# Kernel optimization log

Hardware: AMD Instinct MI355X
Metric: run time of the kernel (lower is better)

The kernel has to match this reference:

```python
import jax, jax.numpy as jnp
import numpy as np

T, D, H, B = 2048, 1152, 16, 8
DH = D // H  # 72


def _apply_rope(x, cos_h, sin_h):
    # x: [T, H, DH]; cos_h, sin_h: [T, DH//2] (already chunked halves)
    c = jnp.concatenate([cos_h, cos_h], axis=-1)[:, None, :]  # [T,1,DH]
    s = jnp.concatenate([sin_h, sin_h], axis=-1)[:, None, :]
    x1, x2 = jnp.split(x, 2, axis=-1)
    rot = jnp.concatenate([-x2, x1], axis=-1)
    return x * c + rot * s


def setup_inputs() -> dict:
    key = jax.random.key(0)
    ks = jax.random.split(key, 12)
    hidden_states = jax.random.normal(ks[0], (T, D), jnp.float32)
    inner = jnp.sort(jax.random.randint(ks[1], (B - 1,), 1, T))
    cu_seqlens = jnp.concatenate(
        [jnp.zeros((1,), jnp.int32), inner.astype(jnp.int32), jnp.full((1,), T, jnp.int32)])
    cos = jax.random.uniform(ks[2], (T, DH), jnp.float32, -1.0, 1.0)
    sin = jax.random.uniform(ks[3], (T, DH), jnp.float32, -1.0, 1.0)
    std = 0.02
    Wq = jax.random.normal(ks[4], (D, D), jnp.float32) * std
    Wk = jax.random.normal(ks[5], (D, D), jnp.float32) * std
    Wv = jax.random.normal(ks[6], (D, D), jnp.float32) * std
    Wo = jax.random.normal(ks[7], (D, D), jnp.float32) * std
    bq = jnp.zeros((D,), jnp.float32)
    bk = jnp.zeros((D,), jnp.float32)
    bv = jnp.zeros((D,), jnp.float32)
    bo = jnp.zeros((D,), jnp.float32)
    return {"hidden_states": hidden_states, "cu_seqlens": cu_seqlens,
            "cos": cos, "sin": sin,
            "Wq": Wq, "bq": bq, "Wk": Wk, "bk": bk,
            "Wv": Wv, "bv": bv, "Wo": Wo, "bo": bo}


def reference(hidden_states, cu_seqlens, cos, sin, Wq, bq, Wk, bk, Wv, bv, Wo, bo):
    t = hidden_states.shape[0]
    scale = DH ** -0.5
    q = (hidden_states @ Wq.T + bq).reshape(t, H, DH)
    k = (hidden_states @ Wk.T + bk).reshape(t, H, DH)
    v = (hidden_states @ Wv.T + bv).reshape(t, H, DH)
    # RoPE: cos/sin [T, DH] are chunked in half along last dim, first half used
    cos_h = cos[:, : DH // 2]
    sin_h = sin[:, : DH // 2]
    q = _apply_rope(q, cos_h, sin_h)
    k = _apply_rope(k, cos_h, sin_h)
    # segment ids from cu_seqlens -> block-diagonal (varlen) attention mask
    pos = jnp.arange(t)
    seg = jnp.searchsorted(cu_seqlens, pos, side='right') - 1  # [T]
    mask = seg[:, None] == seg[None, :]  # [T, T]
    scores = jnp.einsum('thd,shd->hts', q, k) * scale  # [H, T, T]
    scores = jnp.where(mask[None], scores, jnp.float32(-1e30))
    attn = jax.nn.softmax(scores, axis=-1)
    out = jnp.einsum('hts,shd->thd', attn, v).reshape(t, D)
    return out @ Wo.T + bo
```

## Files before the change

kernel.cpp:

```cpp
#include <hip/hip_runtime.h>

#define TT 2048
#define DM 1152
#define NHEAD 16
#define HDIM 72
#define HDP 96
#define HDV 80

typedef __attribute__((ext_vector_type(8))) __bf16 bf16x8;
typedef __attribute__((ext_vector_type(4))) float f32x4;
typedef unsigned short u16;
typedef unsigned int u32;

__device__ inline u16 f2bf(float f){
  u32 u = __builtin_bit_cast(u32, f);
  return (u16)((u + 0x7FFFu + ((u >> 16) & 1u)) >> 16);
}
__device__ inline float bf2f(u16 v){
  return __builtin_bit_cast(float, ((u32)v) << 16);
}
__device__ inline bf16x8 ldb8(const u16* p){
  uint4 u = *(const uint4*)p;
  return __builtin_bit_cast(bf16x8, u);
}
__device__ inline f32x4 mfma16(bf16x8 a, bf16x8 b, f32x4 c){
  return __builtin_amdgcn_mfma_f32_16x16x32_bf16(a, b, c, 0, 0, 0);
}
__device__ inline void gload_lds16(const u16* g, u16* l){
  __builtin_amdgcn_global_load_lds(
      (const __attribute__((address_space(1))) void*)g,
      (__attribute__((address_space(3))) void*)l, 16, 0, 0);
}

__global__ void k_convert(const float* hid, const float* wq, const float* wk,
                          const float* wv, const float* wo, const int* cu,
                          u16* hb, u16* wqb, u16* wkb, u16* wvb, u16* wob,
                          u16* qhb, u16* khb, int* seg)
{
  long i = (long)blockIdx.x * blockDim.x + threadIdx.x;
  const long NHID = (long)TT * DM;
  const long NW = (long)DM * DM;
  const long NCV = NHID + 4*NW;
  if (i < NHID) {
    hb[i] = f2bf(hid[i]);
  } else if (i < NCV) {
    long j = i - NHID;
    int w = (int)(j / NW);
    long o = j - (long)w * NW;
    const float* src = (w==0)?wq:(w==1)?wk:(w==2)?wv:wo;
    u16* dst = (w==0)?wqb:(w==1)?wkb:(w==2)?wvb:wob;
    dst[o] = f2bf(src[o]);
  } else {
    long j = i - NCV;
    const long PER = (long)NHEAD*TT*12;
    int arr = (int)(j / PER);
    long r = j - (long)arr*PER;
    long th = r / 12;
    int c = (int)(r - th*12);
    ((u32*)(arr ? khb : qhb))[th*48 + 36 + c] = 0u;
  }
  if (i < TT) {
    int c = 0;
    for (int e = 0; e < 9; ++e) c += (cu[e] <= (int)i);
    seg[i] = c - 1;
  }
}

__device__ __forceinline__ void gemm128_body(const u16* __restrict__ A,
                                             const u16* __restrict__ W,
                                             const float* __restrict__ bias,
                                             void* out, int mode, float oscale)
{
  __shared__ __align__(16) u16 As[128*32];
  __shared__ __align__(16) u16 Bs[128*32];
  int tid = threadIdx.x;
  int lane = tid & 63, wid = tid >> 6;
  int l15 = lane & 15, quad = lane >> 4;
  int bm = blockIdx.x * 128, bn = blockIdx.y * 128;
  int wm = (wid>>1)*64, wn = (wid&1)*64;
  f32x4 acc[4][4] = {};
  const u16* ga = A + (long)(bm + (tid>>2))*DM + (tid&3)*8;
  const u16* gb = W + (long)(bn + (tid>>2))*DM + (tid&3)*8;
  u16* lA = As + wid*512;
  u16* lB = Bs + wid*512;
  for (int k0 = 0; k0 < DM; k0 += 32) {
    gload_lds16(ga + k0,          lA);
    gload_lds16(ga + k0 + 64*DM,  lA + 2048);
    gload_lds16(gb + k0,          lB);
    gload_lds16(gb + k0 + 64*DM,  lB + 2048);
    __syncthreads();
    bf16x8 af[4], bfr[4];
    for (int i=0;i<4;i++) af[i]  = ldb8(As + (wm + i*16 + l15)*32 + quad*8);
    for (int i=0;i<4;i++) bfr[i] = ldb8(Bs + (wn + i*16 + l15)*32 + quad*8);
    for (int mi=0;mi<4;mi++)
      for (int ni=0;ni<4;ni++)
        acc[mi][ni] = mfma16(af[mi], bfr[ni], acc[mi][ni]);
    __syncthreads();
  }
  for (int ni=0;ni<4;ni++){
    int n = bn + wn + ni*16 + l15;
    float bv_ = bias[n];
    int h = n / HDIM, dh = n - (n / HDIM)*HDIM;
    for (int mi=0;mi<4;mi++){
      int m0 = bm + wm + mi*16 + quad*4;
      for (int r=0;r<4;r++){
        float v = (acc[mi][ni][r] + bv_) * oscale;
        int m = m0 + r;
        if (mode == 0) {
          ((u16*)out)[((long)(h*TT + m))*HDP + dh] = f2bf(v);
        } else {
          ((u16*)out)[((long)(h*HDV + dh))*TT + m] = f2bf(v);
        }
      }
    }
  }
}

__global__ __launch_bounds__(256) void k_gemm_qkv(const u16* __restrict__ A,
    const u16* __restrict__ Wq, const u16* __restrict__ Wk, const u16* __restrict__ Wv,
    const float* __restrict__ bq, const float* __restrict__ bk, const float* __restrict__ bv,
    u16* oq, u16* ok, u16* ov)
{
  const float scale = 0.11785113019775793f;
  int z = blockIdx.z;
  if (z == 0)      gemm128_body(A, Wq, bq, oq, 0, scale);
  else if (z == 1) gemm128_body(A, Wk, bk, ok, 0, 1.0f);
  else             gemm128_body(A, Wv, bv, ov, 2, 1.0f);
}

__global__ __launch_bounds__(256) void k_gemm_o(const u16* __restrict__ A,
    const u16* __restrict__ W, const float* __restrict__ bias, float* out)
{
  __shared__ __align__(16) u16 As[64*32];
  __shared__ __align__(16) u16 Bs[128*32];
  int tid = threadIdx.x;
  int lane = tid & 63, wid = tid >> 6;
  int l15 = lane & 15, quad = lane >> 4;
  int bm = blockIdx.x * 64, bn = blockIdx.y * 128;
  int wm = (wid>>1)*32, wn = (wid&1)*64;
  f32x4 acc[2][4] = {};
  const u16* ga = A + (long)(bm + (tid>>2)/4)*DM + ((tid>>2)%4)*0;
  ga = A + (long)(bm + (tid>>2))*DM + (tid&3)*8;
  const u16* gb = W + (long)(bn + (tid>>2))*DM + (tid&3)*8;
  u16* lA = As + wid*512;
  u16* lB = Bs + wid*512;
  for (int k0 = 0; k0 < DM; k0 += 32) {
    gload_lds16(ga + k0,          lA);
    gload_lds16(gb + k0,          lB);
    gload_lds16(gb + k0 + 64*DM,  lB + 2048);
    __syncthreads();
    bf16x8 af[2], bfr[4];
    for (int i=0;i<2;i++) af[i]  = ldb8(As + (wm + i*16 + l15)*32 + quad*8);
    for (int i=0;i<4;i++) bfr[i] = ldb8(Bs + (wn + i*16 + l15)*32 + quad*8);
    for (int mi=0;mi<2;mi++)
      for (int ni=0;ni<4;ni++)
        acc[mi][ni] = mfma16(af[mi], bfr[ni], acc[mi][ni]);
    __syncthreads();
  }
  for (int ni=0;ni<4;ni++){
    int n = bn + wn + ni*16 + l15;
    float bv_ = bias[n];
    for (int mi=0;mi<2;mi++){
      int m0 = bm + wm + mi*16 + quad*4;
      for (int r=0;r<4;r++)
        out[(long)(m0 + r)*DM + n] = acc[mi][ni][r] + bv_;
    }
  }
}

__global__ void k_rope(u16* qh, u16* kh, const float* __restrict__ cosb,
                       const float* __restrict__ sinb)
{
  int i = blockIdx.x * blockDim.x + threadIdx.x;
  const int total = 2 * NHEAD * TT * 36;
  if (i >= total) return;
  int d = i % 36; int rest = i / 36;
  int t = rest % TT; rest /= TT;
  int h = rest % NHEAD; int qk = rest / NHEAD;
  u16* base = (qk ? kh : qh) + ((long)h*TT + t)*HDP;
  float x1 = bf2f(base[d]), x2 = bf2f(base[d+36]);
  float c = cosb[t*HDIM + d], s = sinb[t*HDIM + d];
  base[d]    = f2bf(x1*c - x2*s);
  base[d+36] = f2bf(x2*c + x1*s);
}

__global__ __launch_bounds__(256) void k_attn(const u16* __restrict__ qh,
                                              const u16* __restrict__ kh,
                                              const u16* __restrict__ vT,
                                              const int* __restrict__ seg,
                                              const int* __restrict__ cu,
                                              u16* __restrict__ ao)
{
  __shared__ __align__(16) u16 Ks[2][64*96];
  __shared__ __align__(16) u16 pbuf[4][16][72];
  int h = blockIdx.y;
  int tid = threadIdx.x, lane = tid & 63, wid = tid >> 6;
  int l15 = lane & 15, quad = lane >> 4;
  int qb0 = blockIdx.x * 64;
  int qbase = qb0 + wid*16;

  const u16* qp = qh + ((long)h*TT + qbase + l15)*HDP + quad*8;
  bf16x8 qf0 = ldb8(qp), qf1 = ldb8(qp+32), qf2 = ldb8(qp+64);
  int segq[4];
  for (int r=0;r<4;r++) segq[r] = seg[qbase + quad*4 + r];
  f32x4 acc[5] = {};
  float lsum[4] = {0.f, 0.f, 0.f, 0.f};

  int seg_lo = seg[qb0], seg_hi = seg[qb0 + 63];
  int s_begin = cu[seg_lo] & ~63;
  int s_end = cu[seg_hi + 1];
  int nt = (s_end - s_begin + 63) >> 6;

  const u16* kbase = kh + (long)h*TT*HDP;

  {
    const u16* gk = kbase + (long)s_begin*HDP + tid*8;
    u16* lK = Ks[0] + wid*512;
    gload_lds16(gk,        lK);
    gload_lds16(gk + 2048, lK + 2048);
    gload_lds16(gk + 4096, lK + 4096);
  }

  for (int it = 0; it < nt; ++it) {
    int s0 = s_begin + it*64;
    int cur = it & 1;
    __syncthreads();
    if (it + 1 < nt) {
      const u16* gk = kbase + (long)(s0 + 64)*HDP + tid*8;
      u16* lK = Ks[cur^1] + wid*512;
      gload_lds16(gk,        lK);
      gload_lds16(gk + 2048, lK + 2048);
      gload_lds16(gk + 4096, lK + 4096);
    }
    f32x4 sc[4] = {};
    for (int j=0;j<4;j++){
      const u16* kp = Ks[cur] + (j*16 + l15)*96 + quad*8;
      sc[j] = mfma16(qf0, ldb8(kp),    sc[j]);
      sc[j] = mfma16(qf1, ldb8(kp+32), sc[j]);
      sc[j] = mfma16(qf2, ldb8(kp+64), sc[j]);
    }
    int sg[4];
    for (int j=0;j<4;j++) sg[j] = seg[s0 + j*16 + l15];
    float p[4][4];
    for (int j=0;j<4;j++)
      for (int r=0;r<4;r++){
        p[j][r] = (sg[j] == segq[r]) ? __expf(sc[j][r]) : 0.f;
        lsum[r] += p[j][r];
      }
    for (int j=0;j<4;j++)
      for (int r=0;r<4;r++)
        pbuf[wid][quad*4+r][j*16+l15] = f2bf(p[j][r]);
    bf16x8 pf0 = ldb8(&pbuf[wid][l15][quad*8]);
    bf16x8 pf1 = ldb8(&pbuf[wid][l15][32 + quad*8]);
    const u16* vp = vT + ((long)h*HDV + l15)*TT + s0 + quad*8;
    for (int n=0;n<5;n++){
      bf16x8 vf0 = ldb8(vp + (long)n*16*TT);
      bf16x8 vf1 = ldb8(vp + (long)n*16*TT + 32);
      acc[n] = mfma16(pf0, vf0, acc[n]);
      acc[n] = mfma16(pf1, vf1, acc[n]);
    }
  }
  for (int off=1; off<16; off<<=1)
    for (int r=0;r<4;r++)
      lsum[r] += __shfl_xor(lsum[r], off, 64);
  float inv[4];
  for (int r=0;r<4;r++) inv[r] = 1.0f / lsum[r];
  for (int n=0;n<5;n++){
    int dh = n*16 + l15;
    if (dh < HDIM){
      for (int r=0;r<4;r++){
        int t = qbase + quad*4 + r;
        ao[(long)t*DM + h*HDIM + dh] = f2bf(acc[n][r] * inv[r]);
      }
    }
  }
}

extern "C" void kernel_launch(void* const* d_in, const int* in_sizes, int n_in,
                              void* d_out, int out_size, void* d_ws, size_t ws_size,
                              hipStream_t stream)
{
  const float* hid  = (const float*)d_in[0];
  const int*   cu   = (const int*)d_in[1];
  const float* cosb = (const float*)d_in[2];
  const float* sinb = (const float*)d_in[3];
  const float* wq   = (const float*)d_in[4];
  const float* bq   = (const float*)d_in[5];
  const float* wk   = (const float*)d_in[6];
  const float* bk   = (const float*)d_in[7];
  const float* wv   = (const float*)d_in[8];
  const float* bv   = (const float*)d_in[9];
  const float* wo   = (const float*)d_in[10];
  const float* bo   = (const float*)d_in[11];

  char* ws = (char*)d_ws;
  u16* hb  = (u16*)ws; ws += (long)TT*DM*2;
  u16* wqb = (u16*)ws; ws += (long)DM*DM*2;
  u16* wkb = (u16*)ws; ws += (long)DM*DM*2;
  u16* wvb = (u16*)ws; ws += (long)DM*DM*2;
  u16* wob = (u16*)ws; ws += (long)DM*DM*2;
  u16* qhb = (u16*)ws; ws += (long)NHEAD*TT*HDP*2;
  u16* khb = (u16*)ws; ws += (long)NHEAD*TT*HDP*2;
  u16* vTb = (u16*)ws; ws += (long)NHEAD*HDV*TT*2;
  u16* aob = (u16*)ws; ws += (long)TT*DM*2;
  int* seg = (int*)ws; ws += (long)TT*4;

  long nconv = (long)TT*DM + 4L*DM*DM + 2L*NHEAD*TT*12;
  k_convert<<<dim3((nconv + 255)/256), 256, 0, stream>>>(
      hid, wq, wk, wv, wo, cu, hb, wqb, wkb, wvb, wob, qhb, khb, seg);

  dim3 gqkv(TT/128, DM/128, 3);
  k_gemm_qkv<<<gqkv, 256, 0, stream>>>(hb, wqb, wkb, wvb, bq, bk, bv, qhb, khb, vTb);

  int nrope = 2*NHEAD*TT*36;
  k_rope<<<dim3((nrope + 255)/256), 256, 0, stream>>>(qhb, khb, cosb, sinb);

  dim3 ga(TT/64, NHEAD);
  k_attn<<<ga, 256, 0, stream>>>(qhb, khb, vTb, seg, cu, aob);

  dim3 go(TT/64, DM/128);
  k_gemm_o<<<go, 256, 0, stream>>>(aob, wob, bo, (float*)d_out);
}
```

Measured before the change: 205.1 us.

## Split attention key range across two blocks and combine partial sums

Attention over the key tiles is split in two halves along a new grid z dimension. Each half writes unnormalized fp32 accumulators and row sums to workspace, and a new combine kernel adds the halves, normalizes, and writes bf16 output. The goal is more blocks in flight and less load imbalance from long segments (512 blocks on a large GPU), in exchange for an extra kernel launch and extra fp32 global traffic. Because no max is subtracted, the two halves can be added directly without rescaling.

```diff
diff --git a/kernel.cpp b/kernel.cpp
--- a/kernel.cpp
+++ b/kernel.cpp
@@ -6,6 +6,7 @@
 #define HDIM 72
 #define HDP 96
 #define HDV 80
+#define KSPLIT 2
 
 typedef __attribute__((ext_vector_type(8))) __bf16 bf16x8;
 typedef __attribute__((ext_vector_type(4))) float f32x4;
@@ -139,8 +140,7 @@
   int bm = blockIdx.x * 64, bn = blockIdx.y * 128;
   int wm = (wid>>1)*32, wn = (wid&1)*64;
   f32x4 acc[2][4] = {};
-  const u16* ga = A + (long)(bm + (tid>>2)/4)*DM + ((tid>>2)%4)*0;
-  ga = A + (long)(bm + (tid>>2))*DM + (tid&3)*8;
+  const u16* ga = A + (long)(bm + (tid>>2))*DM + (tid&3)*8;
   const u16* gb = W + (long)(bn + (tid>>2))*DM + (tid&3)*8;
   u16* lA = As + wid*512;
   u16* lB = Bs + wid*512;
@@ -189,11 +189,13 @@
                                               const u16* __restrict__ vT,
                                               const int* __restrict__ seg,
                                               const int* __restrict__ cu,
-                                              u16* __restrict__ ao)
+                                              float* __restrict__ pacc,
+                                              float* __restrict__ plsum)
 {
   __shared__ __align__(16) u16 Ks[2][64*96];
   __shared__ __align__(16) u16 pbuf[4][16][72];
   int h = blockIdx.y;
+  int z = blockIdx.z;
   int tid = threadIdx.x, lane = tid & 63, wid = tid >> 6;
   int l15 = lane & 15, quad = lane >> 4;
   int qb0 = blockIdx.x * 64;
@@ -210,70 +212,91 @@
   int s_begin = cu[seg_lo] & ~63;
   int s_end = cu[seg_hi + 1];
   int nt = (s_end - s_begin + 63) >> 6;
+  int nt0 = (nt + 1) >> 1;
+  int it_lo = z ? nt0 : 0;
+  int it_hi = z ? nt : nt0;
 
   const u16* kbase = kh + (long)h*TT*HDP;
 
-  {
-    const u16* gk = kbase + (long)s_begin*HDP + tid*8;
-    u16* lK = Ks[0] + wid*512;
-    gload_lds16(gk,        lK);
-    gload_lds16(gk + 2048, lK + 2048);
-    gload_lds16(gk + 4096, lK + 4096);
-  }
-
-  for (int it = 0; it < nt; ++it) {
-    int s0 = s_begin + it*64;
-    int cur = it & 1;
-    __syncthreads();
-    if (it + 1 < nt) {
-      const u16* gk = kbase + (long)(s0 + 64)*HDP + tid*8;
-      u16* lK = Ks[cur^1] + wid*512;
+  if (it_lo < it_hi) {
+    {
+      const u16* gk = kbase + (long)(s_begin + it_lo*64)*HDP + tid*8;
+      u16* lK = Ks[0] + wid*512;
       gload_lds16(gk,        lK);
       gload_lds16(gk + 2048, lK + 2048);
       gload_lds16(gk + 4096, lK + 4096);
     }
-    f32x4 sc[4] = {};
-    for (int j=0;j<4;j++){
-      const u16* kp = Ks[cur] + (j*16 + l15)*96 + quad*8;
-      sc[j] = mfma16(qf0, ldb8(kp),    sc[j]);
-      sc[j] = mfma16(qf1, ldb8(kp+32), sc[j]);
-      sc[j] = mfma16(qf2, ldb8(kp+64), sc[j]);
-    }
-    int sg[4];
-    for (int j=0;j<4;j++) sg[j] = seg[s0 + j*16 + l15];
-    float p[4][4];
-    for (int j=0;j<4;j++)
-      for (int r=0;r<4;r++){
-        p[j][r] = (sg[j] == segq[r]) ? __expf(sc[j][r]) : 0.f;
-        lsum[r] += p[j][r];
+    for (int it = it_lo; it < it_hi; ++it) {
+      int s0 = s_begin + it*64;
+      int cur = (it - it_lo) & 1;
+      __syncthreads();
+      if (it + 1 < it_hi) {
+        const u16* gk = kbase + (long)(s0 + 64)*HDP + tid*8;
+        u16* lK = Ks[cur^1] + wid*512;
+        gload_lds16(gk,        lK);
+        gload_lds16(gk + 2048, lK + 2048);
+        gload_lds16(gk + 4096, lK + 4096);
       }
-    for (int j=0;j<4;j++)
-      for (int r=0;r<4;r++)
-        pbuf[wid][quad*4+r][j*16+l15] = f2bf(p[j][r]);
-    bf16x8 pf0 = ldb8(&pbuf[wid][l15][quad*8]);
-    bf16x8 pf1 = ldb8(&pbuf[wid][l15][32 + quad*8]);
-    const u16* vp = vT + ((long)h*HDV + l15)*TT + s0 + quad*8;
-    for (int n=0;n<5;n++){
-      bf16x8 vf0 = ldb8(vp + (long)n*16*TT);
-      bf16x8 vf1 = ldb8(vp + (long)n*16*TT + 32);
-      acc[n] = mfma16(pf0, vf0, acc[n]);
-      acc[n] = mfma16(pf1, vf1, acc[n]);
+      f32x4 sc[4] = {};
+      for (int j=0;j<4;j++){
+        const u16* kp = Ks[cur] + (j*16 + l15)*96 + quad*8;
+        sc[j] = mfma16(qf0, ldb8(kp),    sc[j]);
+        sc[j] = mfma16(qf1, ldb8(kp+32), sc[j]);
+        sc[j] = mfma16(qf2, ldb8(kp+64), sc[j]);
+      }
+      int sg[4];
+      for (int j=0;j<4;j++) sg[j] = seg[s0 + j*16 + l15];
+      float p[4][4];
+      for (int j=0;j<4;j++)
+        for (int r=0;r<4;r++){
+          p[j][r] = (sg[j] == segq[r]) ? __expf(sc[j][r]) : 0.f;
+          lsum[r] += p[j][r];
+        }
+      for (int j=0;j<4;j++)
+        for (int r=0;r<4;r++)
+          pbuf[wid][quad*4+r][j*16+l15] = f2bf(p[j][r]);
+      bf16x8 pf0 = ldb8(&pbuf[wid][l15][quad*8]);
+      bf16x8 pf1 = ldb8(&pbuf[wid][l15][32 + quad*8]);
+      const u16* vp = vT + ((long)h*HDV + l15)*TT + s0 + quad*8;
+      for (int n=0;n<5;n++){
+        bf16x8 vf0 = ldb8(vp + (long)n*16*TT);
+        bf16x8 vf1 = ldb8(vp + (long)n*16*TT + 32);
+        acc[n] = mfma16(pf0, vf0, acc[n]);
+        acc[n] = mfma16(pf1, vf1, acc[n]);
+      }
     }
   }
   for (int off=1; off<16; off<<=1)
     for (int r=0;r<4;r++)
       lsum[r] += __shfl_xor(lsum[r], off, 64);
-  float inv[4];
-  for (int r=0;r<4;r++) inv[r] = 1.0f / lsum[r];
   for (int n=0;n<5;n++){
     int dh = n*16 + l15;
-    if (dh < HDIM){
-      for (int r=0;r<4;r++){
-        int t = qbase + quad*4 + r;
-        ao[(long)t*DM + h*HDIM + dh] = f2bf(acc[n][r] * inv[r]);
-      }
-    }
-  }
+    for (int r=0;r<4;r++){
+      int t = qbase + quad*4 + r;
+      pacc[(((long)z*TT + t)*NHEAD + h)*HDV + dh] = acc[n][r];
+    }
+  }
+  if (l15 == 0){
+    for (int r=0;r<4;r++){
+      int t = qbase + quad*4 + r;
+      plsum[((long)z*TT + t)*NHEAD + h] = lsum[r];
+    }
+  }
+}
+
+__global__ void k_combine(const float* __restrict__ pacc,
+                          const float* __restrict__ plsum,
+                          u16* __restrict__ ao)
+{
+  int i = blockIdx.x*blockDim.x + threadIdx.x;
+  const int total = TT*NHEAD*HDIM;
+  if (i >= total) return;
+  int dh = i % HDIM; int rest = i / HDIM;
+  int h = rest % NHEAD; int t = rest / NHEAD;
+  long i0 = ((long)t*NHEAD + h)*HDV + dh;
+  float a = pacc[i0] + pacc[(long)TT*NHEAD*HDV + i0];
+  float l = plsum[t*NHEAD + h] + plsum[TT*NHEAD + t*NHEAD + h];
+  ao[(long)t*DM + h*HDIM + dh] = f2bf(a / l);
 }
 
 extern "C" void kernel_launch(void* const* d_in, const int* in_sizes, int n_in,
@@ -304,6 +327,8 @@
   u16* vTb = (u16*)ws; ws += (long)NHEAD*HDV*TT*2;
   u16* aob = (u16*)ws; ws += (long)TT*DM*2;
   int* seg = (int*)ws; ws += (long)TT*4;
+  float* pacc  = (float*)ws; ws += (long)KSPLIT*TT*NHEAD*HDV*4;
+  float* plsum = (float*)ws; ws += (long)KSPLIT*TT*NHEAD*4;
 
   long nconv = (long)TT*DM + 4L*DM*DM + 2L*NHEAD*TT*12;
   k_convert<<<dim3((nconv + 255)/256), 256, 0, stream>>>(
@@ -315,8 +340,11 @@
   int nrope = 2*NHEAD*TT*36;
   k_rope<<<dim3((nrope + 255)/256), 256, 0, stream>>>(qhb, khb, cosb, sinb);
 
-  dim3 ga(TT/64, NHEAD);
-  k_attn<<<ga, 256, 0, stream>>>(qhb, khb, vTb, seg, cu, aob);
+  dim3 ga(TT/64, NHEAD, KSPLIT);
+  k_attn<<<ga, 256, 0, stream>>>(qhb, khb, vTb, seg, cu, pacc, plsum);
+
+  int ncomb = TT*NHEAD*HDIM;
+  k_combine<<<dim3((ncomb + 255)/256), 256, 0, stream>>>(pacc, plsum, aob);
 
   dim3 go(TT/64, DM/128);
   k_gemm_o<<<go, 256, 0, stream>>>(aob, wob, bo, (float*)d_out);
```

Measured after the change: 205.4 us. No clear change (+0.2%).
